# Optimization experiments

Measured on AMD Instinct MI355X. Metric: run time of the kernel, lower is better.

The kernel has to match this reference:

```python
import jax, jax.numpy as jnp
import numpy as np
from jax import lax

# Mamba2 hyperparameters (mamba_ssm defaults scaled to d_model=512)
D_MODEL = 512
EXPAND = 2
D_INNER = EXPAND * D_MODEL          # 1024
HEADDIM = 64
NHEADS = D_INNER // HEADDIM         # 16
D_STATE = 64
NGROUPS = 1
D_CONV = 4
CONV_DIM = D_INNER + 2 * NGROUPS * D_STATE   # 1152
D_IN_PROJ = 2 * D_INNER + 2 * NGROUPS * D_STATE + NHEADS  # 2192
EPS = 1e-5


def setup_inputs() -> dict:
    key = jax.random.key(0)
    ks = jax.random.split(key, 8)
    x = jax.random.normal(ks[0], (4, 2044, D_MODEL), jnp.float32)
    in_proj_w = jax.random.normal(ks[1], (D_MODEL, D_IN_PROJ), jnp.float32) * 0.02
    conv_w = jax.random.normal(ks[2], (CONV_DIM, 1, D_CONV), jnp.float32) * 0.2  # depthwise [O,I/g,K]
    conv_b = jnp.zeros((CONV_DIM,), jnp.float32)
    dt_bias = jax.random.uniform(ks[3], (NHEADS,), jnp.float32, 0.0, 0.1)
    A_log = jnp.log(jax.random.uniform(ks[4], (NHEADS,), jnp.float32, 1.0, 16.0))
    D_skip = jnp.ones((NHEADS,), jnp.float32)
    norm_w = jnp.ones((D_INNER,), jnp.float32)
    out_proj_w = jax.random.normal(ks[5], (D_INNER, D_MODEL), jnp.float32) * 0.02
    return {
        "x": x, "in_proj_w": in_proj_w, "conv_w": conv_w, "conv_b": conv_b,
        "dt_bias": dt_bias, "A_log": A_log, "D_skip": D_skip,
        "norm_w": norm_w, "out_proj_w": out_proj_w,
    }


def _mamba2(x, in_proj_w, conv_w, conv_b, dt_bias, A_log, D_skip, norm_w, out_proj_w):
    B, Lp, _ = x.shape
    zxbcdt = x @ in_proj_w                                  # [B,Lp,D_IN_PROJ]
    z = zxbcdt[..., :D_INNER]                               # gate
    xBC = zxbcdt[..., D_INNER:D_INNER + CONV_DIM]
    dt = zxbcdt[..., D_INNER + CONV_DIM:]                   # [B,Lp,H]

    # causal depthwise conv over time, then silu
    xBC_c = lax.conv_general_dilated(
        xBC.transpose(0, 2, 1), conv_w, window_strides=(1,),
        padding=[(D_CONV - 1, 0)], feature_group_count=CONV_DIM,
        dimension_numbers=("NCH", "OIH", "NCH"))
    xBC = jax.nn.silu(xBC_c.transpose(0, 2, 1) + conv_b)    # [B,Lp,CONV_DIM]

    xs = xBC[..., :D_INNER]
    Bm = xBC[..., D_INNER:D_INNER + NGROUPS * D_STATE]      # [B,Lp,N] (g=1)
    Cm = xBC[..., D_INNER + NGROUPS * D_STATE:]             # [B,Lp,N]

    dt = jax.nn.softplus(dt + dt_bias)                      # [B,Lp,H]
    A = -jnp.exp(A_log)                                     # [H]
    xh = xs.reshape(B, Lp, NHEADS, HEADDIM)                 # [B,Lp,H,P]

    decay = jnp.exp(dt * A)                                 # [B,Lp,H]
    dtx = dt[..., None] * xh                                # [B,Lp,H,P]

    def step(h, inp):
        dec_t, dtx_t, B_t, C_t = inp                        # [B,H],[B,H,P],[B,N],[B,N]
        h = dec_t[:, :, None, None] * h + dtx_t[..., None] * B_t[:, None, None, :]
        y_t = jnp.einsum("bhpn,bn->bhp", h, C_t)
        return h, y_t

    h0 = jnp.zeros((B, NHEADS, HEADDIM, D_STATE), x.dtype)
    _, ys = lax.scan(step, h0, (decay.transpose(1, 0, 2),
                                dtx.transpose(1, 0, 2, 3),
                                Bm.transpose(1, 0, 2),
                                Cm.transpose(1, 0, 2)))
    y = ys.transpose(1, 0, 2, 3) + D_skip[None, None, :, None] * xh  # [B,Lp,H,P]
    y = y.reshape(B, Lp, D_INNER)

    # gated RMSNorm (RMSNormGated): gate first, then normalize
    y = y * jax.nn.silu(z)
    y = y * lax.rsqrt(jnp.mean(y * y, axis=-1, keepdims=True) + EPS) * norm_w
    return y @ out_proj_w                                   # [B,Lp,D_MODEL]


def reference(x, in_proj_w, conv_w, conv_b, dt_bias, A_log, D_skip, norm_w, out_proj_w):
    # MemoryEfficientMamba wrapper: pad seq_len to multiple of 8, run mamba, slice back
    L = x.shape[1]
    pad = (-L) % 8
    xp = jnp.pad(x, ((0, 0), (0, pad), (0, 0))) if pad else x
    out = _mamba2(xp, in_proj_w, conv_w, conv_b, dt_bias, A_log, D_skip, norm_w, out_proj_w)
    return out[:, :L, :]
```

## Files before the change

### kernel.cpp

```cpp
#include <hip/hip_runtime.h>
#include <hip/hip_bf16.h>
#include <math.h>
#include <string.h>

#define BATCH   4
#define SEQ     2044
#define DMODEL  512
#define DINNER  1024
#define NHEADS  16
#define HEADDIM 64
#define DSTATE  64
#define CONVDIM 1152
#define DINPROJ 2192
#define ZW      2176
#define NROWS   (BATCH*SEQ)
#define Q       64
#define NCHUNK  32

typedef __attribute__((ext_vector_type(8))) short bf16x8;
typedef __attribute__((ext_vector_type(4))) float f32x4;

#define MFMA(a,b,c) __builtin_amdgcn_mfma_f32_16x16x32_bf16((a),(b),(c),0,0,0)

__device__ inline short f2bf(float f) {
    __hip_bfloat16 h = __float2bfloat16(f);
    short s; memcpy(&s, &h, 2); return s;
}
__device__ inline float bf2f(short s) {
    unsigned u = ((unsigned)(unsigned short)s) << 16;
    float f; memcpy(&f, &u, 4); return f;
}

__device__ __forceinline__ void gload16(const short* g, short* l) {
    __builtin_amdgcn_global_load_lds(
        (const __attribute__((address_space(1))) void*)g,
        (__attribute__((address_space(3))) void*)l, 16, 0, 0);
}

__global__ __launch_bounds__(256) void convert_bf16_kernel(const float* __restrict__ in,
                                                           short* __restrict__ out, int n8) {
    int i = blockIdx.x * 256 + threadIdx.x;
    if (i >= n8) return;
    float4 v0 = *((const float4*)in + i * 2);
    float4 v1 = *((const float4*)in + i * 2 + 1);
    short t[8];
    t[0]=f2bf(v0.x); t[1]=f2bf(v0.y); t[2]=f2bf(v0.z); t[3]=f2bf(v0.w);
    t[4]=f2bf(v1.x); t[5]=f2bf(v1.y); t[6]=f2bf(v1.z); t[7]=f2bf(v1.w);
    *((bf16x8*)out + i) = *(const bf16x8*)t;
}

__global__ __launch_bounds__(256) void transpose_cvt_kernel(const float* __restrict__ in,
                                                            short* __restrict__ out,
                                                            int R, int Cc, int ldi) {
    __shared__ float tile[64][65];
    const int bx = blockIdx.x * 64;
    const int by = blockIdx.y * 64;
    const int tid = threadIdx.x;
#pragma unroll
    for (int i = 0; i < 16; i++) {
        int idx = tid + i * 256; int r = idx >> 6, c = idx & 63;
        float v = 0.f;
        if (by + r < R && bx + c < Cc) v = in[(size_t)(by + r) * ldi + bx + c];
        tile[r][c] = v;
    }
    __syncthreads();
#pragma unroll
    for (int i = 0; i < 16; i++) {
        int idx = tid + i * 256; int c = idx >> 6, r = idx & 63;
        if (bx + c < Cc && by + r < R)
            out[(size_t)(bx + c) * R + by + r] = f2bf(tile[r][c]);
    }
}

template<bool BF16OUT>
__global__ __launch_bounds__(256) void gemm_bf16(const short* __restrict__ A,
                                                 const short* __restrict__ Bt,
                                                 void* __restrict__ Cv,
                                                 int M, int N, int K,
                                                 int Nbf, float* __restrict__ dtout) {
    __shared__ short As[64][64];
    __shared__ short Bs[64][64];
    const int tid = threadIdx.x;
    const int wave = tid >> 6, lane = tid & 63;
    const int bm = blockIdx.x * 64, bn = blockIdx.y * 64;
    const int lane15 = lane & 15;
    const int kgrp = lane >> 4;
    const int srow = lane >> 3;
    const int scol = (lane & 7) ^ srow;

    f32x4 acc[4];
#pragma unroll
    for (int j = 0; j < 4; j++) acc[j] = (f32x4){0.f, 0.f, 0.f, 0.f};

    const short* Ab = A + (size_t)(bm + wave * 16 + srow) * K + scol * 8;
    const short* Bb = Bt + (size_t)(bn + wave * 16 + srow) * K + scol * 8;
    const int r7 = lane15 & 7;

    for (int kk = 0; kk < K; kk += 64) {
        gload16(Ab + kk,             &As[wave * 16][0]);
        gload16(Ab + 8 * (size_t)K + kk, &As[wave * 16 + 8][0]);
        gload16(Bb + kk,             &Bs[wave * 16][0]);
        gload16(Bb + 8 * (size_t)K + kk, &Bs[wave * 16 + 8][0]);
        __syncthreads();
        const int arow = (wave << 4) + lane15;
        bf16x8 a0 = *(const bf16x8*)&As[arow][(kgrp ^ r7) * 8];
        bf16x8 a1 = *(const bf16x8*)&As[arow][((kgrp + 4) ^ r7) * 8];
#pragma unroll
        for (int j = 0; j < 4; j++) {
            const int brow = (j << 4) + lane15;
            bf16x8 b0 = *(const bf16x8*)&Bs[brow][(kgrp ^ r7) * 8];
            bf16x8 b1 = *(const bf16x8*)&Bs[brow][((kgrp + 4) ^ r7) * 8];
            acc[j] = MFMA(a0, b0, acc[j]);
            acc[j] = MFMA(a1, b1, acc[j]);
        }
        __syncthreads();
    }
    const int crow = bm + (wave << 4) + ((lane >> 4) << 2);
    const int ccol0 = bn + lane15;
    const int ndt = N - Nbf;
#pragma unroll
    for (int j = 0; j < 4; j++) {
        int gn = ccol0 + j * 16;
        if (gn >= N) continue;
#pragma unroll
        for (int i = 0; i < 4; i++) {
            int gm = crow + i;
            if (gm >= M) continue;
            float v = acc[j][i];
            if (BF16OUT) {
                if (dtout != nullptr && gn >= Nbf)
                    dtout[(size_t)gm * ndt + (gn - Nbf)] = v;
                else
                    ((short*)Cv)[(size_t)gm * Nbf + gn] = f2bf(v);
            } else {
                ((float*)Cv)[(size_t)gm * N + gn] = v;
            }
        }
    }
}

__global__ __launch_bounds__(256) void conv_silu_kernel(const short* __restrict__ zxb,
                                                        const float* __restrict__ conv_w,
                                                        const float* __restrict__ conv_b,
                                                        short* __restrict__ convo) {
    int idx = blockIdx.x * 256 + threadIdx.x;
    if (idx >= BATCH * (SEQ/4) * CONVDIM) return;
    int c = idx % CONVDIM;
    int q = idx / CONVDIM;
    int b = q / (SEQ/4);
    int t0 = (q % (SEQ/4)) * 4;
    const size_t base = ((size_t)b * SEQ + t0) * ZW + DINNER + c;
    float4 wv = *(const float4*)&conv_w[c * 4];
    float xv[7];
#pragma unroll
    for (int i = 0; i < 7; i++) {
        int t = t0 - 3 + i;
        xv[i] = (t >= 0) ? bf2f(zxb[base + (size_t)(i - 3) * ZW]) : 0.f;
    }
    const float bias = conv_b[c];
    const size_t obase = ((size_t)b * SEQ + t0) * CONVDIM + c;
#pragma unroll
    for (int i = 0; i < 4; i++) {
        float a = bias + xv[i]*wv.x + xv[i+1]*wv.y + xv[i+2]*wv.z + xv[i+3]*wv.w;
        float s = a / (1.f + expf(-a));
        convo[obase + (size_t)i * CONVDIM] = f2bf(s);
    }
}

__global__ __launch_bounds__(256) void la_kernel(const float* __restrict__ dtraw,
                                                 const float* __restrict__ dt_bias,
                                                 const float* __restrict__ A_log,
                                                 float* __restrict__ la) {
    int idx = blockIdx.x * 256 + threadIdx.x;
    if (idx >= NROWS * NHEADS) return;
    int h = idx & 15;
    float v = dtraw[idx] + dt_bias[h];
    float sp = (v > 20.f) ? v : log1pf(expf(v));
    la[idx] = sp * (-expf(A_log[h]));
}

__global__ __launch_bounds__(256) void chunk_state_kernel(
    const short* __restrict__ convo,
    const float* __restrict__ lab,
    const float* __restrict__ A_log,
    float* __restrict__ Sbuf,
    float* __restrict__ atot)
{
    const int blk = blockIdx.x;
    const int h  = blk & 15;
    const int bc = blk >> 4;
    const int c  = bc & (NCHUNK - 1);
    const int b  = bc >> 5;
    const int t0 = c * Q;
    const int len = min(Q, SEQ - t0);
    const int tid = threadIdx.x;
    const int wave = tid >> 6, lane = tid & 63;
    const size_t rowbase = (size_t)b * SEQ + t0;

    __shared__ short Xt[64][72];
    __shared__ short Bw[64][72];
    __shared__ float sw[64];

    if (tid < 64) {
        const float nAinv = -expf(-A_log[h]);
        float lav = 0.f;
        if (tid < len) lav = lab[(rowbase + tid) * NHEADS + h];
        float dtv = lav * nAinv;
        float v = lav;
#pragma unroll
        for (int off = 1; off < 64; off <<= 1) {
            float nb = __shfl_up(v, off);
            if (lane >= off) v += nb;
        }
        float last = __shfl(v, 63);
        sw[tid] = expf(last - v) * dtv;
        if (tid == 63) atot[blk] = expf(last);
    }
    __syncthreads();

    {
        const int r = tid >> 2, qq = tid & 3;
        const bf16x8 zz = {0,0,0,0,0,0,0,0};
        bf16x8 b0 = zz, b1 = zz, x0 = zz, x1 = zz;
        if (r < len) {
            const short* row = convo + (rowbase + r) * CONVDIM;
            b0 = *(const bf16x8*)&row[1024 + qq*16];
            b1 = *(const bf16x8*)&row[1024 + qq*16 + 8];
            x0 = *(const bf16x8*)&row[h*64 + qq*16];
            x1 = *(const bf16x8*)&row[h*64 + qq*16 + 8];
        }
        const float wsc = sw[r];
        short bs[16], xs[16];
        *(bf16x8*)&bs[0] = b0; *(bf16x8*)&bs[8] = b1;
        *(bf16x8*)&xs[0] = x0; *(bf16x8*)&xs[8] = x1;
#pragma unroll
        for (int i = 0; i < 16; i++) Xt[qq*16+i][r] = xs[i];
#pragma unroll
        for (int i = 0; i < 16; i++) Bw[qq*16+i][r] = f2bf(bf2f(bs[i]) * wsc);
    }
    __syncthreads();

    const int arow = (wave << 4) + (lane & 15);
    const int koff = (lane >> 4) << 3;
    const int trow0 = (wave << 4) + ((lane >> 4) << 2);
    const int scol = lane & 15;

    f32x4 sacc[4];
#pragma unroll
    for (int j = 0; j < 4; j++) sacc[j] = (f32x4){0.f,0.f,0.f,0.f};
    {
        bf16x8 a0 = *(const bf16x8*)&Xt[arow][koff];
        bf16x8 a1 = *(const bf16x8*)&Xt[arow][32 + koff];
#pragma unroll
        for (int j = 0; j < 4; j++) {
            const int brow = (j << 4) + (lane & 15);
            bf16x8 b0 = *(const bf16x8*)&Bw[brow][koff];
            bf16x8 b1 = *(const bf16x8*)&Bw[brow][32 + koff];
            sacc[j] = MFMA(a0, b0, sacc[j]);
            sacc[j] = MFMA(a1, b1, sacc[j]);
        }
    }
    const size_t sbase = (size_t)blk * 4096;
#pragma unroll
    for (int j = 0; j < 4; j++) {
        int n = j * 16 + scol;
#pragma unroll
        for (int i = 0; i < 4; i++) {
            int p = trow0 + i;
            Sbuf[sbase + p * 64 + n] = sacc[j][i];
        }
    }
}

__global__ __launch_bounds__(256) void chunk_state_scan_kernel(
    const float* __restrict__ Sbuf, const float* __restrict__ atot,
    short* __restrict__ Hbf)
{
    int e = blockIdx.x * 256 + threadIdx.x;
    int bh = e >> 12;
    int el = e & 4095;
    int b = bh >> 4, h = bh & 15;
    float H = 0.f;
    for (int c = 0; c < NCHUNK; c++) {
        int blk = (b * NCHUNK + c) * NHEADS + h;
        size_t off = (size_t)blk * 4096 + el;
        Hbf[off] = f2bf(H);
        H = atot[blk] * H + Sbuf[off];
    }
}

__global__ __launch_bounds__(256) void chunk_yfuse_kernel(
    const short* __restrict__ convo,
    const float* __restrict__ lab,
    const float* __restrict__ A_log,
    const float* __restrict__ D_skip,
    const short* __restrict__ Hbf,
    short* __restrict__ ybf)
{
    const int blk = blockIdx.x;
    const int h  = blk & 15;
    const int bc = blk >> 4;
    const int c  = bc & (NCHUNK - 1);
    const int b  = bc >> 5;
    const int t0 = c * Q;
    const int len = min(Q, SEQ - t0);
    const int tid = threadIdx.x;
    const int wave = tid >> 6, lane = tid & 63;
    const size_t rowbase = (size_t)b * SEQ + t0;

    __shared__ short Ct[64][72];
    __shared__ short Bt2[64][72];
    __shared__ short Xt[64][72];
    __shared__ short Hs[64][72];
    __shared__ float cum[64], sdt[64];

    if (tid < 64) {
        const float nAinv = -expf(-A_log[h]);
        float lav = 0.f;
        if (tid < len) lav = lab[(rowbase + tid) * NHEADS + h];
        float dtv = lav * nAinv;
        float v = lav;
#pragma unroll
        for (int off = 1; off < 64; off <<= 1) {
            float nb = __shfl_up(v, off);
            if (lane >= off) v += nb;
        }
        cum[tid] = v; sdt[tid] = dtv;
    }
    __syncthreads();

    {
        const int r = tid >> 2, qq = tid & 3;
        const bf16x8 zz = {0,0,0,0,0,0,0,0};
        bf16x8 c0 = zz, c1 = zz, b0 = zz, b1 = zz, x0 = zz, x1 = zz;
        if (r < len) {
            const short* row = convo + (rowbase + r) * CONVDIM;
            c0 = *(const bf16x8*)&row[1088 + qq*16];
            c1 = *(const bf16x8*)&row[1088 + qq*16 + 8];
            b0 = *(const bf16x8*)&row[1024 + qq*16];
            b1 = *(const bf16x8*)&row[1024 + qq*16 + 8];
            x0 = *(const bf16x8*)&row[h*64 + qq*16];
            x1 = *(const bf16x8*)&row[h*64 + qq*16 + 8];
        }
        *(bf16x8*)&Ct[r][qq*16]    = c0; *(bf16x8*)&Ct[r][qq*16+8]  = c1;
        *(bf16x8*)&Bt2[r][qq*16]   = b0; *(bf16x8*)&Bt2[r][qq*16+8] = b1;
        short xs[16];
        *(bf16x8*)&xs[0] = x0; *(bf16x8*)&xs[8] = x1;
#pragma unroll
        for (int i = 0; i < 16; i++) Xt[qq*16+i][r] = xs[i];
        const size_t hbase = (size_t)blk * 4096;
        bf16x8 h0 = *(const bf16x8*)&Hbf[hbase + r*64 + qq*16];
        bf16x8 h1 = *(const bf16x8*)&Hbf[hbase + r*64 + qq*16 + 8];
        *(bf16x8*)&Hs[r][qq*16]   = h0;
        *(bf16x8*)&Hs[r][qq*16+8] = h1;
    }
    __syncthreads();

    const int arow = (wave << 4) + (lane & 15);
    const int koff = (lane >> 4) << 3;
    const int trow0 = (wave << 4) + ((lane >> 4) << 2);
    const int scol = lane & 15;

    f32x4 eacc[4], iacc[4];
#pragma unroll
    for (int j = 0; j < 4; j++) { eacc[j] = (f32x4){0.f,0.f,0.f,0.f}; iacc[j] = (f32x4){0.f,0.f,0.f,0.f}; }
    {
        bf16x8 a0 = *(const bf16x8*)&Ct[arow][koff];
        bf16x8 a1 = *(const bf16x8*)&Ct[arow][32 + koff];
#pragma unroll
        for (int j = 0; j < 4; j++) {
            const int brow = (j << 4) + (lane & 15);
            bf16x8 b0 = *(const bf16x8*)&Bt2[brow][koff];
            bf16x8 b1 = *(const bf16x8*)&Bt2[brow][32 + koff];
            eacc[j] = MFMA(a0, b0, eacc[j]);
            eacc[j] = MFMA(a1, b1, eacc[j]);
            bf16x8 h0 = *(const bf16x8*)&Hs[brow][koff];
            bf16x8 h1 = *(const bf16x8*)&Hs[brow][32 + koff];
            iacc[j] = MFMA(a0, h0, iacc[j]);
            iacc[j] = MFMA(a1, h1, iacc[j]);
        }
    }
    short ebf[4][4];
#pragma unroll
    for (int j = 0; j < 4; j++) {
        int s = j * 16 + scol;
#pragma unroll
        for (int i = 0; i < 4; i++) {
            int t = trow0 + i;
            float val = 0.f;
            if (s <= t) val = eacc[j][i] * expf(cum[t] - cum[s]) * sdt[s];
            ebf[j][i] = f2bf(val);
        }
    }
    __syncthreads();
#pragma unroll
    for (int j = 0; j < 4; j++)
#pragma unroll
        for (int i = 0; i < 4; i++)
            Ct[trow0 + i][j * 16 + scol] = ebf[j][i];
    __syncthreads();

    f32x4 yacc[4];
#pragma unroll
    for (int j = 0; j < 4; j++) yacc[j] = (f32x4){0.f,0.f,0.f,0.f};
    {
        bf16x8 a0 = *(const bf16x8*)&Ct[arow][koff];
        bf16x8 a1 = *(const bf16x8*)&Ct[arow][32 + koff];
#pragma unroll
        for (int j = 0; j < 4; j++) {
            const int brow = (j << 4) + (lane & 15);
            bf16x8 b0 = *(const bf16x8*)&Xt[brow][koff];
            bf16x8 b1 = *(const bf16x8*)&Xt[brow][32 + koff];
            yacc[j] = MFMA(a0, b0, yacc[j]);
            yacc[j] = MFMA(a1, b1, yacc[j]);
        }
    }
    const float dsk = D_skip[h];
#pragma unroll
    for (int j = 0; j < 4; j++) {
        int p = j * 16 + scol;
#pragma unroll
        for (int i = 0; i < 4; i++) {
            int t = trow0 + i;
            if (t < len) {
                float ce = expf(cum[t]);
                float xv = bf2f(Xt[p][t]);
                float val = yacc[j][i] + ce * iacc[j][i] + dsk * xv;
                ybf[(rowbase + t) * DINNER + h * 64 + p] = f2bf(val);
            }
        }
    }
}

__global__ __launch_bounds__(256) void gate_rmsnorm_kernel(short* __restrict__ y,
                                                           const short* __restrict__ zxb,
                                                           const float* __restrict__ norm_w) {
    const int m = blockIdx.x;
    const int tid = threadIdx.x;
    float vals[4];
    float ss = 0.f;
#pragma unroll
    for (int i = 0; i < 4; i++) {
        int c = tid + i * 256;
        float v = bf2f(y[(size_t)m * DINNER + c]);
        float z = bf2f(zxb[(size_t)m * ZW + c]);
        float g = v * (z / (1.f + expf(-z)));
        vals[i] = g;
        ss += g * g;
    }
#pragma unroll
    for (int mask = 1; mask < 64; mask <<= 1) ss += __shfl_xor(ss, mask);
    __shared__ float red[4];
    if ((tid & 63) == 0) red[tid >> 6] = ss;
    __syncthreads();
    float tot = red[0] + red[1] + red[2] + red[3];
    float scale = rsqrtf(tot / 1024.f + 1e-5f);
#pragma unroll
    for (int i = 0; i < 4; i++) {
        int c = tid + i * 256;
        float r = vals[i] * scale * norm_w[c];
        y[(size_t)m * DINNER + c] = f2bf(r);
    }
}

extern "C" void kernel_launch(void* const* d_in, const int* in_sizes, int n_in,
                              void* d_out, int out_size, void* d_ws, size_t ws_size,
                              hipStream_t stream) {
    const float* x          = (const float*)d_in[0];
    const float* in_proj_w  = (const float*)d_in[1];
    const float* conv_w     = (const float*)d_in[2];
    const float* conv_b     = (const float*)d_in[3];
    const float* dt_bias    = (const float*)d_in[4];
    const float* A_log      = (const float*)d_in[5];
    const float* D_skip     = (const float*)d_in[6];
    const float* norm_w     = (const float*)d_in[7];
    const float* out_proj_w = (const float*)d_in[8];
    float* out = (float*)d_out;

    short* zxb   = (short*)d_ws;
    short* convo = zxb + (size_t)NROWS * ZW;
    short* ybf   = convo + (size_t)NROWS * CONVDIM;
    short* Hbf   = ybf + (size_t)NROWS * DINNER;
    float* lab   = (float*)(Hbf + (size_t)2048 * 4096);
    float* dtraw = lab + (size_t)NROWS * NHEADS;
    float* Sbuf  = dtraw + (size_t)NROWS * NHEADS;
    float* atotb = Sbuf + (size_t)2048 * 4096;
    short* w2t   = (short*)(atotb + 2048);
    short* xb  = convo;
    short* w1t = xb + (size_t)NROWS * DMODEL;

    convert_bf16_kernel<<<(NROWS * DMODEL / 8 + 255) / 256, 256, 0, stream>>>(x, xb, NROWS * DMODEL / 8);
    {
        dim3 g((DINPROJ + 63) / 64, (DMODEL + 63) / 64);
        transpose_cvt_kernel<<<g, 256, 0, stream>>>(in_proj_w, w1t, DMODEL, DINPROJ, DINPROJ);
    }
    {
        dim3 g((DMODEL + 63) / 64, (DINNER + 63) / 64);
        transpose_cvt_kernel<<<g, 256, 0, stream>>>(out_proj_w, w2t, DINNER, DMODEL, DMODEL);
    }

    {
        dim3 g((NROWS + 63) / 64, (DINPROJ + 63) / 64);
        gemm_bf16<true><<<g, 256, 0, stream>>>(xb, w1t, zxb, NROWS, DINPROJ, DMODEL, ZW, dtraw);
    }

    {
        int tot = BATCH * (SEQ / 4) * CONVDIM;
        conv_silu_kernel<<<(tot + 255) / 256, 256, 0, stream>>>(zxb, conv_w, conv_b, convo);
    }

    la_kernel<<<(NROWS * NHEADS + 255) / 256, 256, 0, stream>>>(dtraw, dt_bias, A_log, lab);

    chunk_state_kernel<<<BATCH * NCHUNK * NHEADS, 256, 0, stream>>>(
        convo, lab, A_log, Sbuf, atotb);

    chunk_state_scan_kernel<<<(64 * 4096) / 256, 256, 0, stream>>>(Sbuf, atotb, Hbf);

    chunk_yfuse_kernel<<<BATCH * NCHUNK * NHEADS, 256, 0, stream>>>(
        convo, lab, A_log, D_skip, Hbf, ybf);

    gate_rmsnorm_kernel<<<NROWS, 256, 0, stream>>>(ybf, zxb, norm_w);

    {
        dim3 g((NROWS + 63) / 64, (DMODEL + 63) / 64);
        gemm_bf16<false><<<g, 256, 0, stream>>>(ybf, w2t, out, NROWS, DMODEL, DINNER, DMODEL, nullptr);
    }
}
```

Measured before the change: 145.9 us.

## Double-buffer GEMM LDS, fuse dt softplus into GEMM epilogue, store chunk states bf16

The GEMM now double-buffers its shared-memory A/B tiles, so the next k-tile's loads are issued before the current tile's MFMAs and one barrier per iteration is dropped. The softplus(dt+bias)*(-exp(A_log)) computation moves into the in-projection GEMM epilogue, which removes the separate la_kernel launch and its dtraw round trip. Per-chunk states are stored as bf16 instead of fp32, halving that buffer's traffic at some cost in precision for the inter-chunk scan. Double buffering doubles LDS use per block, which may lower occupancy.

```diff
diff --git a/kernel.cpp b/kernel.cpp
--- a/kernel.cpp
+++ b/kernel.cpp
@@ -77,9 +77,11 @@
                                                  const short* __restrict__ Bt,
                                                  void* __restrict__ Cv,
                                                  int M, int N, int K,
-                                                 int Nbf, float* __restrict__ dtout) {
-    __shared__ short As[64][64];
-    __shared__ short Bs[64][64];
+                                                 int Nbf, float* __restrict__ dtout,
+                                                 const float* __restrict__ dt_bias,
+                                                 const float* __restrict__ A_log) {
+    __shared__ short As[2][64][64];
+    __shared__ short Bs[2][64][64];
     const int tid = threadIdx.x;
     const int wave = tid >> 6, lane = tid & 63;
     const int bm = blockIdx.x * 64, bn = blockIdx.y * 64;
@@ -87,6 +89,7 @@
     const int kgrp = lane >> 4;
     const int srow = lane >> 3;
     const int scol = (lane & 7) ^ srow;
+    const int r7 = lane15 & 7;
 
     f32x4 acc[4];
 #pragma unroll
@@ -94,27 +97,39 @@
 
     const short* Ab = A + (size_t)(bm + wave * 16 + srow) * K + scol * 8;
     const short* Bb = Bt + (size_t)(bn + wave * 16 + srow) * K + scol * 8;
-    const int r7 = lane15 & 7;
-
-    for (int kk = 0; kk < K; kk += 64) {
-        gload16(Ab + kk,             &As[wave * 16][0]);
-        gload16(Ab + 8 * (size_t)K + kk, &As[wave * 16 + 8][0]);
-        gload16(Bb + kk,             &Bs[wave * 16][0]);
-        gload16(Bb + 8 * (size_t)K + kk, &Bs[wave * 16 + 8][0]);
-        __syncthreads();
+
+    gload16(Ab,                 &As[0][wave * 16][0]);
+    gload16(Ab + 8 * (size_t)K, &As[0][wave * 16 + 8][0]);
+    gload16(Bb,                 &Bs[0][wave * 16][0]);
+    gload16(Bb + 8 * (size_t)K, &Bs[0][wave * 16 + 8][0]);
+    __syncthreads();
+
+    const int nk = K >> 6;
+    int cur = 0;
+    for (int s = 0; s < nk; s++) {
+        if (s + 1 < nk) {
+            const int kk = (s + 1) << 6;
+            const int nxt = cur ^ 1;
+            gload16(Ab + kk,                 &As[nxt][wave * 16][0]);
+            gload16(Ab + 8 * (size_t)K + kk, &As[nxt][wave * 16 + 8][0]);
+            gload16(Bb + kk,                 &Bs[nxt][wave * 16][0]);
+            gload16(Bb + 8 * (size_t)K + kk, &Bs[nxt][wave * 16 + 8][0]);
+        }
         const int arow = (wave << 4) + lane15;
-        bf16x8 a0 = *(const bf16x8*)&As[arow][(kgrp ^ r7) * 8];
-        bf16x8 a1 = *(const bf16x8*)&As[arow][((kgrp + 4) ^ r7) * 8];
+        bf16x8 a0 = *(const bf16x8*)&As[cur][arow][(kgrp ^ r7) * 8];
+        bf16x8 a1 = *(const bf16x8*)&As[cur][arow][((kgrp + 4) ^ r7) * 8];
 #pragma unroll
         for (int j = 0; j < 4; j++) {
             const int brow = (j << 4) + lane15;
-            bf16x8 b0 = *(const bf16x8*)&Bs[brow][(kgrp ^ r7) * 8];
-            bf16x8 b1 = *(const bf16x8*)&Bs[brow][((kgrp + 4) ^ r7) * 8];
+            bf16x8 b0 = *(const bf16x8*)&Bs[cur][brow][(kgrp ^ r7) * 8];
+            bf16x8 b1 = *(const bf16x8*)&Bs[cur][brow][((kgrp + 4) ^ r7) * 8];
             acc[j] = MFMA(a0, b0, acc[j]);
             acc[j] = MFMA(a1, b1, acc[j]);
         }
         __syncthreads();
-    }
+        cur ^= 1;
+    }
+
     const int crow = bm + (wave << 4) + ((lane >> 4) << 2);
     const int ccol0 = bn + lane15;
     const int ndt = N - Nbf;
@@ -128,10 +143,14 @@
             if (gm >= M) continue;
             float v = acc[j][i];
             if (BF16OUT) {
-                if (dtout != nullptr && gn >= Nbf)
-                    dtout[(size_t)gm * ndt + (gn - Nbf)] = v;
-                else
+                if (dtout != nullptr && gn >= Nbf) {
+                    int h = gn - Nbf;
+                    float v2 = v + dt_bias[h];
+                    float sp = (v2 > 20.f) ? v2 : log1pf(expf(v2));
+                    dtout[(size_t)gm * ndt + h] = sp * (-expf(A_log[h]));
+                } else {
                     ((short*)Cv)[(size_t)gm * Nbf + gn] = f2bf(v);
+                }
             } else {
                 ((float*)Cv)[(size_t)gm * N + gn] = v;
             }
@@ -167,23 +186,11 @@
     }
 }
 
-__global__ __launch_bounds__(256) void la_kernel(const float* __restrict__ dtraw,
-                                                 const float* __restrict__ dt_bias,
-                                                 const float* __restrict__ A_log,
-                                                 float* __restrict__ la) {
-    int idx = blockIdx.x * 256 + threadIdx.x;
-    if (idx >= NROWS * NHEADS) return;
-    int h = idx & 15;
-    float v = dtraw[idx] + dt_bias[h];
-    float sp = (v > 20.f) ? v : log1pf(expf(v));
-    la[idx] = sp * (-expf(A_log[h]));
-}
-
 __global__ __launch_bounds__(256) void chunk_state_kernel(
     const short* __restrict__ convo,
     const float* __restrict__ lab,
     const float* __restrict__ A_log,
-    float* __restrict__ Sbuf,
+    short* __restrict__ Sbf,
     float* __restrict__ atot)
 {
     const int blk = blockIdx.x;
@@ -267,13 +274,13 @@
 #pragma unroll
         for (int i = 0; i < 4; i++) {
             int p = trow0 + i;
-            Sbuf[sbase + p * 64 + n] = sacc[j][i];
+            Sbf[sbase + p * 64 + n] = f2bf(sacc[j][i]);
         }
     }
 }
 
 __global__ __launch_bounds__(256) void chunk_state_scan_kernel(
-    const float* __restrict__ Sbuf, const float* __restrict__ atot,
+    const short* __restrict__ Sbf, const float* __restrict__ atot,
     short* __restrict__ Hbf)
 {
     int e = blockIdx.x * 256 + threadIdx.x;
@@ -285,7 +292,7 @@
         int blk = (b * NCHUNK + c) * NHEADS + h;
         size_t off = (size_t)blk * 4096 + el;
         Hbf[off] = f2bf(H);
-        H = atot[blk] * H + Sbuf[off];
+        H = atot[blk] * H + bf2f(Sbf[off]);
     }
 }
 
@@ -481,10 +488,9 @@
     short* convo = zxb + (size_t)NROWS * ZW;
     short* ybf   = convo + (size_t)NROWS * CONVDIM;
     short* Hbf   = ybf + (size_t)NROWS * DINNER;
-    float* lab   = (float*)(Hbf + (size_t)2048 * 4096);
-    float* dtraw = lab + (size_t)NROWS * NHEADS;
-    float* Sbuf  = dtraw + (size_t)NROWS * NHEADS;
-    float* atotb = Sbuf + (size_t)2048 * 4096;
+    short* Sbf   = Hbf + (size_t)2048 * 4096;
+    float* lab   = (float*)(Sbf + (size_t)2048 * 4096);
+    float* atotb = lab + (size_t)NROWS * NHEADS;
     short* w2t   = (short*)(atotb + 2048);
     short* xb  = convo;
     short* w1t = xb + (size_t)NROWS * DMODEL;
@@ -501,7 +507,8 @@
 
     {
         dim3 g((NROWS + 63) / 64, (DINPROJ + 63) / 64);
-        gemm_bf16<true><<<g, 256, 0, stream>>>(xb, w1t, zxb, NROWS, DINPROJ, DMODEL, ZW, dtraw);
+        gemm_bf16<true><<<g, 256, 0, stream>>>(xb, w1t, zxb, NROWS, DINPROJ, DMODEL,
+                                               ZW, lab, dt_bias, A_log);
     }
 
     {
@@ -509,12 +516,10 @@
         conv_silu_kernel<<<(tot + 255) / 256, 256, 0, stream>>>(zxb, conv_w, conv_b, convo);
     }
 
-    la_kernel<<<(NROWS * NHEADS + 255) / 256, 256, 0, stream>>>(dtraw, dt_bias, A_log, lab);
-
     chunk_state_kernel<<<BATCH * NCHUNK * NHEADS, 256, 0, stream>>>(
-        convo, lab, A_log, Sbuf, atotb);
-
-    chunk_state_scan_kernel<<<(64 * 4096) / 256, 256, 0, stream>>>(Sbuf, atotb, Hbf);
+        convo, lab, A_log, Sbf, atotb);
+
+    chunk_state_scan_kernel<<<(64 * 4096) / 256, 256, 0, stream>>>(Sbf, atotb, Hbf);
 
     chunk_yfuse_kernel<<<BATCH * NCHUNK * NHEADS, 256, 0, stream>>>(
         convo, lab, A_log, D_skip, Hbf, ybf);
@@ -523,6 +528,7 @@
 
     {
         dim3 g((NROWS + 63) / 64, (DMODEL + 63) / 64);
-        gemm_bf16<false><<<g, 256, 0, stream>>>(ybf, w2t, out, NROWS, DMODEL, DINNER, DMODEL, nullptr);
-    }
-}
+        gemm_bf16<false><<<g, 256, 0, stream>>>(ybf, w2t, out, NROWS, DMODEL, DINNER,
+                                                DMODEL, nullptr, nullptr, nullptr);
+    }
+}
```

Result: slower. 149.5 us (+2.5%).
